# Kernel optimization log

Hardware: AMD Instinct MI355X
Metric: run time of the kernel (lower is better)

## Reference

```python
import jax, jax.numpy as jnp
import numpy as np

NUM_PER_SCALE = (64, 64, 64)   # static num_intervals_per_scale
DIST_BINS = 21
NUM_CLASSES = 5
D = 128   # node_embedding_dim
N = 512   # number of nodes (time frames)
KSIZE = 5


def _gru_last(x_seq, lens, Wih, Whh, bih, bhh):
    """Masked GRU over padded seqs; final hidden at each sequence's true length.
    x_seq: [I, T, F], lens: [I]. PyTorch GRU cell math."""
    I, T, _ = x_seq.shape
    H = Whh.shape[1]
    mask_t = (jnp.arange(T)[None, :] < lens[:, None]).T  # [T, I]

    def step(h, inp):
        x_t, m = inp
        gi = x_t @ Wih.T + bih            # [I, 3H]
        gh = h @ Whh.T + bhh
        ir, iz, in_ = jnp.split(gi, 3, axis=-1)
        hr, hz, hn = jnp.split(gh, 3, axis=-1)
        r = jax.nn.sigmoid(ir + hr)
        z = jax.nn.sigmoid(iz + hz)
        n = jnp.tanh(in_ + r * hn)
        h_new = (1.0 - z) * n + z * h
        return jnp.where(m[:, None], h_new, h), None

    h0 = jnp.zeros((I, H), x_seq.dtype)
    h_fin, _ = jax.lax.scan(step, h0, (jnp.swapaxes(x_seq, 0, 1), mask_t))
    return h_fin


def _bigru_last(x_pad, lens, Wih, Whh, bih, bhh):
    """Bidirectional GRU final hiddens, matching packed-sequence semantics."""
    hf = _gru_last(x_pad, lens, Wih[0], Whh[0], bih[0], bhh[0])
    T = x_pad.shape[1]
    t = jnp.arange(T)[None, :]
    rev = jnp.where(t < lens[:, None], lens[:, None] - 1 - t, t)  # reverse within valid length
    x_rev = jnp.take_along_axis(x_pad, rev[:, :, None], axis=1)
    hb = _gru_last(x_rev, lens, Wih[1], Whh[1], bih[1], bhh[1])
    return hf, hb


def reference(node_embeddings, time_positions, node_pred, audio_len,
              cur_anchor_intervals, smooth_kernel,
              feat_Wih, feat_Whh, feat_bih, feat_bhh,
              abn_Wih, abn_Whh, abn_bih, abn_bhh,
              start_w, end_w,
              uni_W1, uni_b1, uni_W2, uni_b2, uni_W3, uni_b3):
    n, d = node_embeddings.shape
    al = audio_len
    # temporal encoding
    freqs = jnp.linspace(0.0, 10.0, d)
    x = node_embeddings + 0.05 * jnp.sin(time_positions * freqs)  # [N, D]
    # grouped gaussian smoothing over time per class channel (symmetric kernel)
    pad = KSIZE // 2
    xp = jnp.pad(node_pred, ((pad, pad), (0, 0)))
    win = jnp.stack([xp[k:k + n] for k in range(KSIZE)])          # [K, N, C]
    smoothed = jax.nn.softmax(jnp.einsum('k,knc->nc', smooth_kernel, win), axis=-1)
    abnormal = smoothed[:, 0]                                     # normal_class_idx = 0
    tpos = time_positions[:, 0] * al                              # [N]

    bounds_list, conf_list, cls_list = [], [], []
    off = 0
    for s in range(3):
        ni = NUM_PER_SCALE[s]
        anc = cur_anchor_intervals[off:off + ni]
        off += ni
        starts, ends = anc[:, 0], anc[:, 1]
        mask = (tpos[None, :] >= starts[:, None]) & (tpos[None, :] <= ends[:, None])  # [ni, N]
        lens = mask.sum(axis=1)
        # stable gather: in-interval nodes first, original node order preserved
        key = jnp.where(mask, 0, n) + jnp.arange(n)[None, :]
        order = jnp.argsort(key, axis=1)
        x_pad = x[order]                       # [ni, N, D]
        abn_pad = abnormal[order][:, :, None]  # [ni, N, 1]
        hf, hb = _bigru_last(x_pad, lens, feat_Wih[s], feat_Whh[s], feat_bih[s], feat_bhh[s])
        af, ab = _bigru_last(abn_pad, lens, abn_Wih[s], abn_Whh[s], abn_bih[s], abn_bhh[s])
        local_feat = jnp.concatenate([hf, hb], axis=1)             # [ni, 2D]
        local_abn = (af[:, 0] + ab[:, 0]) * 0.5
        centers = (starts + ends) * 0.5
        widths = ends - starts
        sf = jnp.concatenate([local_feat, local_abn[:, None],
                              (centers / al)[:, None], (widths / al)[:, None]], axis=1)
        h = jax.nn.relu(sf @ uni_W1[s] + uni_b1[s])
        h = jax.nn.relu(h @ uni_W2[s] + uni_b2[s])   # dropout inactive (eval)
        out = h @ uni_W3[s] + uni_b3[s]
        sl = out[:, :DIST_BINS]
        el = out[:, DIST_BINS:2 * DIST_BINS]
        conf = out[:, 2 * DIST_BINS]
        cls = out[:, 2 * DIST_BINS + 1:]
        so = jax.nn.softmax(sl, axis=1) @ start_w[s]
        eo = jax.nn.softmax(el, axis=1) @ end_w[s]
        st = jnp.clip(starts + so, 0.0, al)
        en = jnp.clip(ends + eo, 0.0, al)
        bounds_list.append(jnp.stack([st, en], axis=1))
        conf_list.append(conf)
        cls_list.append(cls)
    return (jnp.concatenate(bounds_list, 0),
            jnp.concatenate(conf_list, 0),
            jnp.concatenate(cls_list, 0))


def setup_inputs():
    key = jax.random.key(0)
    ks = jax.random.split(key, 16)
    node_embeddings = jax.random.normal(ks[0], (N, D), dtype=jnp.float32)
    time_positions = jax.random.uniform(ks[1], (N, 1), dtype=jnp.float32)
    node_pred = jax.random.normal(ks[2], (N, NUM_CLASSES), dtype=jnp.float32)
    audio_len = jnp.ones((), jnp.float32)
    total = sum(NUM_PER_SCALE)
    st = jax.random.uniform(ks[3], (total,), minval=0.0, maxval=0.75)
    wd = jax.random.uniform(ks[4], (total,), minval=0.05, maxval=0.2)
    cur_anchor_intervals = jnp.stack([st, jnp.minimum(st + wd, 1.0)], axis=1)
    smooth_kernel = jnp.array([0.06136, 0.24477, 0.38774, 0.24477, 0.06136], jnp.float32)
    feat_Wih = 0.05 * jax.random.normal(ks[5], (3, 2, 3 * D, D))
    feat_Whh = 0.05 * jax.random.normal(ks[6], (3, 2, 3 * D, D))
    feat_bih = 0.05 * jax.random.normal(ks[7], (3, 2, 3 * D))
    feat_bhh = 0.05 * jax.random.normal(ks[8], (3, 2, 3 * D))
    abn_Wih = 0.5 * jax.random.normal(ks[9], (3, 2, 3, 1))
    abn_Whh = 0.5 * jax.random.normal(ks[10], (3, 2, 3, 1))
    abn_bih = 0.5 * jax.random.normal(ks[11], (3, 2, 3))
    abn_bhh = 0.5 * jax.random.normal(ks[12], (3, 2, 3))
    lin = jnp.linspace(-20.0, 20.0, DIST_BINS)
    start_w = jnp.tile(lin[None, :], (3, 1))
    end_w = jnp.tile(lin[None, :], (3, 1))
    fin = 2 * D + 3
    fout = 2 * DIST_BINS + 1 + (NUM_CLASSES - 1)
    uni_W1 = jax.random.normal(ks[13], (3, fin, 256)) / float(np.sqrt(fin))
    uni_b1 = jnp.zeros((3, 256), jnp.float32)
    uni_W2 = jax.random.normal(ks[14], (3, 256, 256)) / 16.0
    uni_b2 = jnp.zeros((3, 256), jnp.float32)
    uni_W3 = jax.random.normal(ks[15], (3, 256, fout)) / 16.0
    uni_b3 = jnp.zeros((3, fout), jnp.float32)
    return dict(node_embeddings=node_embeddings, time_positions=time_positions,
                node_pred=node_pred, audio_len=audio_len,
                cur_anchor_intervals=cur_anchor_intervals, smooth_kernel=smooth_kernel,
                feat_Wih=feat_Wih, feat_Whh=feat_Whh, feat_bih=feat_bih, feat_bhh=feat_bhh,
                abn_Wih=abn_Wih, abn_Whh=abn_Whh, abn_bih=abn_bih, abn_bhh=abn_bhh,
                start_w=start_w, end_w=end_w,
                uni_W1=uni_W1, uni_b1=uni_b1, uni_W2=uni_W2, uni_b2=uni_b2,
                uni_W3=uni_W3, uni_b3=uni_b3)
```

## Files before the change

kernel.cpp:

```cpp
#include <hip/hip_runtime.h>
#include <math.h>

#define N_NODES 512
#define DIM 128
#define NANCH 192
#define G3 384
#define FOUT 47
#define DBINS 21

__device__ __forceinline__ float fast_sigmoid(float x) {
    return __builtin_amdgcn_rcpf(1.f + __expf(-x));
}
__device__ __forceinline__ float fast_tanh(float x) {
    return 1.f - 2.f * __builtin_amdgcn_rcpf(1.f + __expf(2.f * x));
}

__global__ __launch_bounds__(384) void prep_kernel(
    const float* __restrict__ emb, const float* __restrict__ tpin,
    const float* __restrict__ Wih, const float* __restrict__ bih,
    const float* __restrict__ alp, const float* __restrict__ anchors,
    const float* __restrict__ npred, const float* __restrict__ skern,
    const float* __restrict__ aWih, const float* __restrict__ aWhh,
    const float* __restrict__ abih, const float* __restrict__ abhh,
    float* __restrict__ xW, int* __restrict__ members,
    int* __restrict__ lens, float* __restrict__ abn_res)
{
    int blk = blockIdx.x;
    int tid = threadIdx.x;
    if (blk < 192) {
        int sd = blk >> 5;
        int ng = blk & 31;
        __shared__ __align__(16) float xs[16][DIM];
        for (int idx = tid; idx < 16 * DIM; idx += 384) {
            int m = idx >> 7, k = idx & 127;
            int node = ng * 16 + m;
            float tv = tpin[node];
            float freq = 10.f * (float)k / 127.f;
            xs[m][k] = emb[node * DIM + k] + 0.05f * __sinf(tv * freq);
        }
        __syncthreads();
        float acc[16];
        float b = bih[sd * G3 + tid];
        #pragma unroll
        for (int m = 0; m < 16; ++m) acc[m] = b;
        const float* wrow = Wih + ((size_t)sd * G3 + tid) * DIM;
        for (int k = 0; k < DIM; k += 4) {
            float4 w4 = *(const float4*)(wrow + k);
            #pragma unroll
            for (int m = 0; m < 16; ++m) {
                float4 xv = *(const float4*)&xs[m][k];
                acc[m] = fmaf(w4.x, xv.x, acc[m]);
                acc[m] = fmaf(w4.y, xv.y, acc[m]);
                acc[m] = fmaf(w4.z, xv.z, acc[m]);
                acc[m] = fmaf(w4.w, xv.w, acc[m]);
            }
        }
        #pragma unroll
        for (int m = 0; m < 16; ++m)
            xW[((size_t)sd * N_NODES + ng * 16 + m) * G3 + tid] = acc[m];
    } else {
        int a = blk - 192;
        float al = alp[0];
        float s0 = anchors[a * 2 + 0];
        float e0 = anchors[a * 2 + 1];
        __shared__ int memloc[N_NODES];
        __shared__ float abn_lds[N_NODES];
        for (int node = tid; node < N_NODES; node += 384) {
            float sc[5];
            #pragma unroll
            for (int ch = 0; ch < 5; ++ch) {
                float acc = 0.f;
                #pragma unroll
                for (int k = 0; k < 5; ++k) {
                    int r = node + k - 2;
                    if (r >= 0 && r < N_NODES) acc += skern[k] * npred[r * 5 + ch];
                }
                sc[ch] = acc;
            }
            float m = sc[0];
            #pragma unroll
            for (int ch = 1; ch < 5; ++ch) m = fmaxf(m, sc[ch]);
            float sum = 0.f;
            #pragma unroll
            for (int ch = 0; ch < 5; ++ch) sum += __expf(sc[ch] - m);
            abn_lds[node] = __expf(sc[0] - m) / sum;
        }
        __syncthreads();
        if (tid < 64) {
            int lane = tid;
            int count = 0;
            for (int c = 0; c < N_NODES / 64; ++c) {
                int node = c * 64 + lane;
                float tp = tpin[node] * al;
                bool in = (tp >= s0) && (tp <= e0);
                unsigned long long m = __ballot(in);
                if (in) {
                    int pos = count + __popcll(m & ((1ull << lane) - 1ull));
                    members[a * N_NODES + pos] = node;
                    memloc[pos] = node;
                }
                count += __popcll(m);
            }
            if (lane == 0) lens[a] = count;
            int sc3 = a >> 6;
            float h = 0.f;
            if (lane < 2) {
                int sd = sc3 * 2 + lane;
                float wi0 = aWih[sd*3+0], wi1 = aWih[sd*3+1], wi2 = aWih[sd*3+2];
                float wh0 = aWhh[sd*3+0], wh1 = aWhh[sd*3+1], wh2 = aWhh[sd*3+2];
                float bi0 = abih[sd*3+0], bi1 = abih[sd*3+1], bi2 = abih[sd*3+2];
                float bh0 = abhh[sd*3+0], bh1 = abhh[sd*3+1], bh2 = abhh[sd*3+2];
                for (int t = 0; t < count; ++t) {
                    int idx = lane ? (count - 1 - t) : t;
                    float xv = abn_lds[memloc[idx]];
                    float r = fast_sigmoid(fmaf(wi0, xv, bi0) + fmaf(wh0, h, bh0));
                    float z = fast_sigmoid(fmaf(wi1, xv, bi1) + fmaf(wh1, h, bh1));
                    float nv = fast_tanh(fmaf(wi2, xv, bi2) + r * fmaf(wh2, h, bh2));
                    h = (1.f - z) * nv + z * h;
                }
            }
            float hb = __shfl(h, 1);
            if (lane == 0) abn_res[a] = 0.5f * (h + hb);
        }
    }
}

__global__ __launch_bounds__(512, 2) void gru_feat_kernel(
    const float* __restrict__ xW, const float* __restrict__ Whh,
    const float* __restrict__ bhh, const int* __restrict__ members,
    const int* __restrict__ lens, float* __restrict__ feat_out)
{
    int b = blockIdx.x;
    int a = b >> 1;
    int dir = b & 1;
    int s3 = a >> 6;
    int sd = s3 * 2 + dir;
    int t0 = threadIdx.x;
    int j  = t0 >> 2;
    int s  = t0 & 3;

    float wr[32], wz[32], wn[32];
    {
        const float* base = Whh + ((size_t)sd * G3) * DIM;
        const float* pr = base + (size_t)(j        ) * DIM + s * 32;
        const float* pz = base + (size_t)(j + DIM  ) * DIM + s * 32;
        const float* pn = base + (size_t)(j + 2*DIM) * DIM + s * 32;
        #pragma unroll
        for (int q = 0; q < 8; ++q) {
            float4 v = *(const float4*)(pr + 4 * q);
            wr[4*q+0]=v.x; wr[4*q+1]=v.y; wr[4*q+2]=v.z; wr[4*q+3]=v.w;
        }
        #pragma unroll
        for (int q = 0; q < 8; ++q) {
            float4 v = *(const float4*)(pz + 4 * q);
            wz[4*q+0]=v.x; wz[4*q+1]=v.y; wz[4*q+2]=v.z; wz[4*q+3]=v.w;
        }
        #pragma unroll
        for (int q = 0; q < 8; ++q) {
            float4 v = *(const float4*)(pn + 4 * q);
            wn[4*q+0]=v.x; wn[4*q+1]=v.y; wn[4*q+2]=v.z; wn[4*q+3]=v.w;
        }
    }
    float bhr = bhh[sd * G3 + j];
    float bhz = bhh[sd * G3 + DIM + j];
    float bhn = bhh[sd * G3 + 2 * DIM + j];

    const float* xWp = xW + (size_t)sd * N_NODES * G3;
    const int* mem = members + a * N_NODES;
    int len = lens[a];

    __shared__ __align__(16) float hbuf[2][4][36];
    for (int i = t0; i < 2 * 4 * 36; i += 512) ((float*)hbuf)[i] = 0.f;
    __syncthreads();

    int node0 = (len > 0) ? mem[dir ? (len - 1) : 0] : 0;
    float gr = xWp[(size_t)node0 * G3 + j];
    float gz = xWp[(size_t)node0 * G3 + DIM + j];
    float gn = xWp[(size_t)node0 * G3 + 2 * DIM + j];

    int cur = 0;
    for (int t = 0; t < len; ++t) {
        float gr_n = 0.f, gz_n = 0.f, gn_n = 0.f;
        if (t + 1 < len) {
            int nn = mem[dir ? (len - 2 - t) : (t + 1)];
            gr_n = xWp[(size_t)nn * G3 + j];
            gz_n = xWp[(size_t)nn * G3 + DIM + j];
            gn_n = xWp[(size_t)nn * G3 + 2 * DIM + j];
        }
        float ar = 0.f, az = 0.f, an_ = 0.f;
        const float4* hp = (const float4*)(&hbuf[cur][s][0]);
        #pragma unroll
        for (int q = 0; q < 8; ++q) {
            float4 hv = hp[q];
            ar = fmaf(wr[4*q+0], hv.x, ar); ar = fmaf(wr[4*q+1], hv.y, ar);
            ar = fmaf(wr[4*q+2], hv.z, ar); ar = fmaf(wr[4*q+3], hv.w, ar);
            az = fmaf(wz[4*q+0], hv.x, az); az = fmaf(wz[4*q+1], hv.y, az);
            az = fmaf(wz[4*q+2], hv.z, az); az = fmaf(wz[4*q+3], hv.w, az);
            an_ = fmaf(wn[4*q+0], hv.x, an_); an_ = fmaf(wn[4*q+1], hv.y, an_);
            an_ = fmaf(wn[4*q+2], hv.z, an_); an_ = fmaf(wn[4*q+3], hv.w, an_);
        }
        ar  += __shfl_xor(ar, 1);  ar  += __shfl_xor(ar, 2);
        az  += __shfl_xor(az, 1);  az  += __shfl_xor(az, 2);
        an_ += __shfl_xor(an_, 1); an_ += __shfl_xor(an_, 2);

        float r  = fast_sigmoid(gr + ar + bhr);
        float z  = fast_sigmoid(gz + az + bhz);
        float nv = fast_tanh(gn + r * (an_ + bhn));
        float hj = hbuf[cur][j >> 5][j & 31];
        float hnew = (1.f - z) * nv + z * hj;
        if (s == 0) hbuf[cur ^ 1][j >> 5][j & 31] = hnew;
        __syncthreads();
        cur ^= 1;
        gr = gr_n; gz = gz_n; gn = gn_n;
    }
    if (s == 0) feat_out[a * 256 + dir * DIM + j] = hbuf[cur][j >> 5][j & 31];
}

__global__ __launch_bounds__(256) void head_kernel(
    const float* __restrict__ feat, const float* __restrict__ abn_res,
    const float* __restrict__ anchors, const float* __restrict__ alp,
    const float* __restrict__ W1, const float* __restrict__ b1,
    const float* __restrict__ W2, const float* __restrict__ b2,
    const float* __restrict__ W3, const float* __restrict__ b3,
    const float* __restrict__ sw, const float* __restrict__ ew,
    float* __restrict__ out)
{
    int a = blockIdx.x;
    int tid = threadIdx.x;
    int s = a >> 6;
    __shared__ float sf[260];
    __shared__ float h1[256];
    __shared__ float h2[256];
    __shared__ float o[FOUT];
    float al = alp[0];
    float st = anchors[a * 2 + 0];
    float en = anchors[a * 2 + 1];
    sf[tid] = feat[a * 256 + tid];
    if (tid == 0) {
        sf[256] = abn_res[a];
        sf[257] = (st + en) * 0.5f / al;
        sf[258] = (en - st) / al;
    }
    __syncthreads();

    const float* w1 = W1 + (size_t)s * 259 * 256;
    float acc = b1[s * 256 + tid];
    for (int jj = 0; jj < 259; ++jj) acc = fmaf(sf[jj], w1[jj * 256 + tid], acc);
    h1[tid] = fmaxf(acc, 0.f);
    __syncthreads();

    const float* w2 = W2 + (size_t)s * 256 * 256;
    acc = b2[s * 256 + tid];
    for (int jj = 0; jj < 256; ++jj) acc = fmaf(h1[jj], w2[jj * 256 + tid], acc);
    h2[tid] = fmaxf(acc, 0.f);
    __syncthreads();

    if (tid < FOUT) {
        const float* w3 = W3 + (size_t)s * 256 * FOUT;
        acc = b3[s * FOUT + tid];
        for (int jj = 0; jj < 256; ++jj) acc = fmaf(h2[jj], w3[jj * FOUT + tid], acc);
        o[tid] = acc;
    }
    __syncthreads();

    if (tid < 2) {
        const float* lw = (tid == 0) ? (sw + s * DBINS) : (ew + s * DBINS);
        const float* sl = o + tid * DBINS;
        float m = sl[0];
        for (int jj = 1; jj < DBINS; ++jj) m = fmaxf(m, sl[jj]);
        float sum = 0.f, dot = 0.f;
        for (int jj = 0; jj < DBINS; ++jj) {
            float e = __expf(sl[jj] - m);
            sum += e;
            dot = fmaf(e, lw[jj], dot);
        }
        float off = dot / sum;
        float base = (tid == 0) ? st : en;
        out[a * 2 + tid] = fminf(fmaxf(base + off, 0.f), al);
    }
    if (tid == 42) out[2 * NANCH + a] = o[42];
    if (tid >= 43 && tid < FOUT) out[3 * NANCH + a * 4 + (tid - 43)] = o[tid];
}

extern "C" void kernel_launch(void* const* d_in, const int* in_sizes, int n_in,
                              void* d_out, int out_size, void* d_ws, size_t ws_size,
                              hipStream_t stream) {
    const float* emb   = (const float*)d_in[0];
    const float* tpin  = (const float*)d_in[1];
    const float* npred = (const float*)d_in[2];
    const float* alp   = (const float*)d_in[3];
    const float* anch  = (const float*)d_in[4];
    const float* skern = (const float*)d_in[5];
    const float* fWih  = (const float*)d_in[6];
    const float* fWhh  = (const float*)d_in[7];
    const float* fbih  = (const float*)d_in[8];
    const float* fbhh  = (const float*)d_in[9];
    const float* aWih  = (const float*)d_in[10];
    const float* aWhh  = (const float*)d_in[11];
    const float* abih  = (const float*)d_in[12];
    const float* abhh  = (const float*)d_in[13];
    const float* sw    = (const float*)d_in[14];
    const float* ew    = (const float*)d_in[15];
    const float* W1    = (const float*)d_in[16];
    const float* b1    = (const float*)d_in[17];
    const float* W2    = (const float*)d_in[18];
    const float* b2    = (const float*)d_in[19];
    const float* W3    = (const float*)d_in[20];
    const float* b3    = (const float*)d_in[21];

    float* ws = (float*)d_ws;
    float* xW       = ws;
    float* abn_res  = ws + 1179648;
    float* feat     = ws + 1179904;
    int*   members  = (int*)(ws + 1229056);
    int*   lens     = (int*)(ws + 1327360);
    float* outp     = (float*)d_out;

    prep_kernel<<<384, 384, 0, stream>>>(emb, tpin, fWih, fbih, alp, anch, npred, skern,
                                         aWih, aWhh, abih, abhh,
                                         xW, members, lens, abn_res);
    gru_feat_kernel<<<2 * NANCH, 512, 0, stream>>>(xW, fWhh, fbhh, members, lens, feat);
    head_kernel<<<NANCH, 256, 0, stream>>>(feat, abn_res, anch, alp,
                                           W1, b1, W2, b2, W3, b3, sw, ew, outp);
}
```

Measured before the change: 252.4 us.

## Process two anchors per GRU block to reuse recurrent weights in registers

Each GRU block now runs two anchor sequences (same scale and direction) together, reusing the register-resident Whh weights for both hidden-state matvecs. This halves the grid to 192 blocks and gives each thread more independent FMA chains, while member index lists are staged into shared memory. The loop runs to the longer of the two lengths and masks updates for the shorter one, so the two lengths going unequal wastes work. The halved block count may also leave many compute units idle.

```diff
diff --git a/kernel.cpp b/kernel.cpp
--- a/kernel.cpp
+++ b/kernel.cpp
@@ -131,89 +131,131 @@
     const int* __restrict__ lens, float* __restrict__ feat_out)
 {
     int b = blockIdx.x;
-    int a = b >> 1;
+    int pr = b >> 1;
     int dir = b & 1;
-    int s3 = a >> 6;
+    int aA = pr * 2, aB = aA + 1;
+    int s3 = aA >> 6;
     int sd = s3 * 2 + dir;
     int t0 = threadIdx.x;
     int j  = t0 >> 2;
     int s  = t0 & 3;
 
+    __shared__ __align__(16) float hbuf[2][2][4][36];
+    __shared__ int memA[N_NODES], memB[N_NODES];
+
+    int lenA = lens[aA], lenB = lens[aB];
+    int len = max(lenA, lenB);
+    for (int i = t0; i < 2 * 2 * 4 * 36; i += 512) ((float*)hbuf)[i] = 0.f;
+    for (int i = t0; i < lenA; i += 512) memA[i] = members[aA * N_NODES + i];
+    for (int i = t0; i < lenB; i += 512) memB[i] = members[aB * N_NODES + i];
+
     float wr[32], wz[32], wn[32];
     {
         const float* base = Whh + ((size_t)sd * G3) * DIM;
-        const float* pr = base + (size_t)(j        ) * DIM + s * 32;
-        const float* pz = base + (size_t)(j + DIM  ) * DIM + s * 32;
-        const float* pn = base + (size_t)(j + 2*DIM) * DIM + s * 32;
+        const float* pr_ = base + (size_t)(j        ) * DIM + s * 32;
+        const float* pz_ = base + (size_t)(j + DIM  ) * DIM + s * 32;
+        const float* pn_ = base + (size_t)(j + 2*DIM) * DIM + s * 32;
         #pragma unroll
         for (int q = 0; q < 8; ++q) {
-            float4 v = *(const float4*)(pr + 4 * q);
+            float4 v = *(const float4*)(pr_ + 4 * q);
             wr[4*q+0]=v.x; wr[4*q+1]=v.y; wr[4*q+2]=v.z; wr[4*q+3]=v.w;
         }
         #pragma unroll
         for (int q = 0; q < 8; ++q) {
-            float4 v = *(const float4*)(pz + 4 * q);
+            float4 v = *(const float4*)(pz_ + 4 * q);
             wz[4*q+0]=v.x; wz[4*q+1]=v.y; wz[4*q+2]=v.z; wz[4*q+3]=v.w;
         }
         #pragma unroll
         for (int q = 0; q < 8; ++q) {
-            float4 v = *(const float4*)(pn + 4 * q);
+            float4 v = *(const float4*)(pn_ + 4 * q);
             wn[4*q+0]=v.x; wn[4*q+1]=v.y; wn[4*q+2]=v.z; wn[4*q+3]=v.w;
         }
     }
     float bhr = bhh[sd * G3 + j];
     float bhz = bhh[sd * G3 + DIM + j];
     float bhn = bhh[sd * G3 + 2 * DIM + j];
-
     const float* xWp = xW + (size_t)sd * N_NODES * G3;
-    const int* mem = members + a * N_NODES;
-    int len = lens[a];
-
-    __shared__ __align__(16) float hbuf[2][4][36];
-    for (int i = t0; i < 2 * 4 * 36; i += 512) ((float*)hbuf)[i] = 0.f;
-    __syncthreads();
-
-    int node0 = (len > 0) ? mem[dir ? (len - 1) : 0] : 0;
-    float gr = xWp[(size_t)node0 * G3 + j];
-    float gz = xWp[(size_t)node0 * G3 + DIM + j];
-    float gn = xWp[(size_t)node0 * G3 + 2 * DIM + j];
+    __syncthreads();
+
+    int nA = (lenA > 0) ? memA[dir ? (lenA - 1) : 0] : 0;
+    int nB = (lenB > 0) ? memB[dir ? (lenB - 1) : 0] : 0;
+    float grA = xWp[(size_t)nA * G3 + j];
+    float gzA = xWp[(size_t)nA * G3 + DIM + j];
+    float gnA = xWp[(size_t)nA * G3 + 2 * DIM + j];
+    float grB = xWp[(size_t)nB * G3 + j];
+    float gzB = xWp[(size_t)nB * G3 + DIM + j];
+    float gnB = xWp[(size_t)nB * G3 + 2 * DIM + j];
 
     int cur = 0;
-    for (int t = 0; t < len; ++t) {
-        float gr_n = 0.f, gz_n = 0.f, gn_n = 0.f;
-        if (t + 1 < len) {
-            int nn = mem[dir ? (len - 2 - t) : (t + 1)];
-            gr_n = xWp[(size_t)nn * G3 + j];
-            gz_n = xWp[(size_t)nn * G3 + DIM + j];
-            gn_n = xWp[(size_t)nn * G3 + 2 * DIM + j];
-        }
-        float ar = 0.f, az = 0.f, an_ = 0.f;
-        const float4* hp = (const float4*)(&hbuf[cur][s][0]);
+    for (int tt = 0; tt < len; ++tt) {
+        float grA_n = 0.f, gzA_n = 0.f, gnA_n = 0.f;
+        float grB_n = 0.f, gzB_n = 0.f, gnB_n = 0.f;
+        int t1 = tt + 1;
+        if (t1 < lenA) {
+            int nn = memA[dir ? (lenA - 1 - t1) : t1];
+            grA_n = xWp[(size_t)nn * G3 + j];
+            gzA_n = xWp[(size_t)nn * G3 + DIM + j];
+            gnA_n = xWp[(size_t)nn * G3 + 2 * DIM + j];
+        }
+        if (t1 < lenB) {
+            int nn = memB[dir ? (lenB - 1 - t1) : t1];
+            grB_n = xWp[(size_t)nn * G3 + j];
+            gzB_n = xWp[(size_t)nn * G3 + DIM + j];
+            gnB_n = xWp[(size_t)nn * G3 + 2 * DIM + j];
+        }
+        float arA = 0.f, azA = 0.f, anA = 0.f;
+        float arB = 0.f, azB = 0.f, anB = 0.f;
+        const float4* hpA = (const float4*)(&hbuf[cur][0][s][0]);
+        const float4* hpB = (const float4*)(&hbuf[cur][1][s][0]);
         #pragma unroll
         for (int q = 0; q < 8; ++q) {
-            float4 hv = hp[q];
-            ar = fmaf(wr[4*q+0], hv.x, ar); ar = fmaf(wr[4*q+1], hv.y, ar);
-            ar = fmaf(wr[4*q+2], hv.z, ar); ar = fmaf(wr[4*q+3], hv.w, ar);
-            az = fmaf(wz[4*q+0], hv.x, az); az = fmaf(wz[4*q+1], hv.y, az);
-            az = fmaf(wz[4*q+2], hv.z, az); az = fmaf(wz[4*q+3], hv.w, az);
-            an_ = fmaf(wn[4*q+0], hv.x, an_); an_ = fmaf(wn[4*q+1], hv.y, an_);
-            an_ = fmaf(wn[4*q+2], hv.z, an_); an_ = fmaf(wn[4*q+3], hv.w, an_);
-        }
-        ar  += __shfl_xor(ar, 1);  ar  += __shfl_xor(ar, 2);
-        az  += __shfl_xor(az, 1);  az  += __shfl_xor(az, 2);
-        an_ += __shfl_xor(an_, 1); an_ += __shfl_xor(an_, 2);
-
-        float r  = fast_sigmoid(gr + ar + bhr);
-        float z  = fast_sigmoid(gz + az + bhz);
-        float nv = fast_tanh(gn + r * (an_ + bhn));
-        float hj = hbuf[cur][j >> 5][j & 31];
-        float hnew = (1.f - z) * nv + z * hj;
-        if (s == 0) hbuf[cur ^ 1][j >> 5][j & 31] = hnew;
+            float4 hA = hpA[q];
+            float4 hB = hpB[q];
+            arA = fmaf(wr[4*q+0], hA.x, arA); arB = fmaf(wr[4*q+0], hB.x, arB);
+            arA = fmaf(wr[4*q+1], hA.y, arA); arB = fmaf(wr[4*q+1], hB.y, arB);
+            arA = fmaf(wr[4*q+2], hA.z, arA); arB = fmaf(wr[4*q+2], hB.z, arB);
+            arA = fmaf(wr[4*q+3], hA.w, arA); arB = fmaf(wr[4*q+3], hB.w, arB);
+            azA = fmaf(wz[4*q+0], hA.x, azA); azB = fmaf(wz[4*q+0], hB.x, azB);
+            azA = fmaf(wz[4*q+1], hA.y, azA); azB = fmaf(wz[4*q+1], hB.y, azB);
+            azA = fmaf(wz[4*q+2], hA.z, azA); azB = fmaf(wz[4*q+2], hB.z, azB);
+            azA = fmaf(wz[4*q+3], hA.w, azA); azB = fmaf(wz[4*q+3], hB.w, azB);
+            anA = fmaf(wn[4*q+0], hA.x, anA); anB = fmaf(wn[4*q+0], hB.x, anB);
+            anA = fmaf(wn[4*q+1], hA.y, anA); anB = fmaf(wn[4*q+1], hB.y, anB);
+            anA = fmaf(wn[4*q+2], hA.z, anA); anB = fmaf(wn[4*q+2], hB.z, anB);
+            anA = fmaf(wn[4*q+3], hA.w, anA); anB = fmaf(wn[4*q+3], hB.w, anB);
+        }
+        arA += __shfl_xor(arA, 1); arA += __shfl_xor(arA, 2);
+        azA += __shfl_xor(azA, 1); azA += __shfl_xor(azA, 2);
+        anA += __shfl_xor(anA, 1); anA += __shfl_xor(anA, 2);
+        arB += __shfl_xor(arB, 1); arB += __shfl_xor(arB, 2);
+        azB += __shfl_xor(azB, 1); azB += __shfl_xor(azB, 2);
+        anB += __shfl_xor(anB, 1); anB += __shfl_xor(anB, 2);
+
+        float rA  = fast_sigmoid(grA + arA + bhr);
+        float zA  = fast_sigmoid(gzA + azA + bhz);
+        float nvA = fast_tanh(gnA + rA * (anA + bhn));
+        float hjA = hbuf[cur][0][j >> 5][j & 31];
+        float hA2 = (tt < lenA) ? ((1.f - zA) * nvA + zA * hjA) : hjA;
+
+        float rB  = fast_sigmoid(grB + arB + bhr);
+        float zB  = fast_sigmoid(gzB + azB + bhz);
+        float nvB = fast_tanh(gnB + rB * (anB + bhn));
+        float hjB = hbuf[cur][1][j >> 5][j & 31];
+        float hB2 = (tt < lenB) ? ((1.f - zB) * nvB + zB * hjB) : hjB;
+
+        if (s == 0) {
+            hbuf[cur ^ 1][0][j >> 5][j & 31] = hA2;
+            hbuf[cur ^ 1][1][j >> 5][j & 31] = hB2;
+        }
         __syncthreads();
         cur ^= 1;
-        gr = gr_n; gz = gz_n; gn = gn_n;
-    }
-    if (s == 0) feat_out[a * 256 + dir * DIM + j] = hbuf[cur][j >> 5][j & 31];
+        grA = grA_n; gzA = gzA_n; gnA = gnA_n;
+        grB = grB_n; gzB = gzB_n; gnB = gnB_n;
+    }
+    if (s == 0) {
+        feat_out[aA * 256 + dir * DIM + j] = hbuf[cur][0][j >> 5][j & 31];
+        feat_out[aB * 256 + dir * DIM + j] = hbuf[cur][1][j >> 5][j & 31];
+    }
 }
 
 __global__ __launch_bounds__(256) void head_kernel(
@@ -319,7 +361,7 @@
     prep_kernel<<<384, 384, 0, stream>>>(emb, tpin, fWih, fbih, alp, anch, npred, skern,
                                          aWih, aWhh, abih, abhh,
                                          xW, members, lens, abn_res);
-    gru_feat_kernel<<<2 * NANCH, 512, 0, stream>>>(xW, fWhh, fbhh, members, lens, feat);
+    gru_feat_kernel<<<NANCH, 512, 0, stream>>>(xW, fWhh, fbhh, members, lens, feat);
     head_kernel<<<NANCH, 256, 0, stream>>>(feat, abn_res, anch, alp,
                                            W1, b1, W2, b2, W3, b3, sw, ew, outp);
 }
```

New measurement: 283.7 us. 12.4% more time.

## Fuse MLP head into GRU kernel via last-block-done atomic flag

Applied to the files above, without the earlier changes.

Removes the separate head kernel launch: each GRU block increments a per-anchor counter after writing its direction's hidden state, and the second block to finish for an anchor runs the three-layer MLP head and output writes. Flags are reset in the prep kernel. This saves a kernel launch and the gap between launches. In exchange it adds threadfences and an atomic, and makes the last-finishing block do serial head work while other blocks may already be done.

```diff
diff --git a/kernel.cpp b/kernel.cpp
--- a/kernel.cpp
+++ b/kernel.cpp
@@ -23,7 +23,8 @@
     const float* __restrict__ aWih, const float* __restrict__ aWhh,
     const float* __restrict__ abih, const float* __restrict__ abhh,
     float* __restrict__ xW, int* __restrict__ members,
-    int* __restrict__ lens, float* __restrict__ abn_res)
+    int* __restrict__ lens, float* __restrict__ abn_res,
+    int* __restrict__ flags)
 {
     int blk = blockIdx.x;
     int tid = threadIdx.x;
@@ -60,6 +61,7 @@
             xW[((size_t)sd * N_NODES + ng * 16 + m) * G3 + tid] = acc[m];
     } else {
         int a = blk - 192;
+        if (tid == 0) flags[a] = 0;
         float al = alp[0];
         float s0 = anchors[a * 2 + 0];
         float e0 = anchors[a * 2 + 1];
@@ -128,7 +130,14 @@
 __global__ __launch_bounds__(512, 2) void gru_feat_kernel(
     const float* __restrict__ xW, const float* __restrict__ Whh,
     const float* __restrict__ bhh, const int* __restrict__ members,
-    const int* __restrict__ lens, float* __restrict__ feat_out)
+    const int* __restrict__ lens, float* __restrict__ feat_out,
+    int* __restrict__ flags, const float* __restrict__ abn_res,
+    const float* __restrict__ anchors, const float* __restrict__ alp,
+    const float* __restrict__ W1, const float* __restrict__ b1,
+    const float* __restrict__ W2, const float* __restrict__ b2,
+    const float* __restrict__ W3, const float* __restrict__ b3,
+    const float* __restrict__ sw, const float* __restrict__ ew,
+    float* __restrict__ out)
 {
     int b = blockIdx.x;
     int a = b >> 1;
@@ -214,20 +223,17 @@
         gr = gr_n; gz = gz_n; gn = gn_n;
     }
     if (s == 0) feat_out[a * 256 + dir * DIM + j] = hbuf[cur][j >> 5][j & 31];
-}
-
-__global__ __launch_bounds__(256) void head_kernel(
-    const float* __restrict__ feat, const float* __restrict__ abn_res,
-    const float* __restrict__ anchors, const float* __restrict__ alp,
-    const float* __restrict__ W1, const float* __restrict__ b1,
-    const float* __restrict__ W2, const float* __restrict__ b2,
-    const float* __restrict__ W3, const float* __restrict__ b3,
-    const float* __restrict__ sw, const float* __restrict__ ew,
-    float* __restrict__ out)
-{
-    int a = blockIdx.x;
-    int tid = threadIdx.x;
-    int s = a >> 6;
+
+    __syncthreads();
+    __shared__ int winner;
+    if (t0 == 0) {
+        __threadfence();
+        winner = atomicAdd(&flags[a], 1);
+    }
+    __syncthreads();
+    if (winner != 1) return;
+    __threadfence();
+
     __shared__ float sf[260];
     __shared__ float h1[256];
     __shared__ float h2[256];
@@ -235,37 +241,38 @@
     float al = alp[0];
     float st = anchors[a * 2 + 0];
     float en = anchors[a * 2 + 1];
-    sf[tid] = feat[a * 256 + tid];
-    if (tid == 0) {
+    if (t0 < 256) sf[t0] = feat_out[a * 256 + t0];
+    if (t0 == 0) {
         sf[256] = abn_res[a];
         sf[257] = (st + en) * 0.5f / al;
         sf[258] = (en - st) / al;
     }
     __syncthreads();
 
-    const float* w1 = W1 + (size_t)s * 259 * 256;
-    float acc = b1[s * 256 + tid];
-    for (int jj = 0; jj < 259; ++jj) acc = fmaf(sf[jj], w1[jj * 256 + tid], acc);
-    h1[tid] = fmaxf(acc, 0.f);
-    __syncthreads();
-
-    const float* w2 = W2 + (size_t)s * 256 * 256;
-    acc = b2[s * 256 + tid];
-    for (int jj = 0; jj < 256; ++jj) acc = fmaf(h1[jj], w2[jj * 256 + tid], acc);
-    h2[tid] = fmaxf(acc, 0.f);
-    __syncthreads();
-
-    if (tid < FOUT) {
-        const float* w3 = W3 + (size_t)s * 256 * FOUT;
-        acc = b3[s * FOUT + tid];
-        for (int jj = 0; jj < 256; ++jj) acc = fmaf(h2[jj], w3[jj * FOUT + tid], acc);
-        o[tid] = acc;
-    }
-    __syncthreads();
-
-    if (tid < 2) {
-        const float* lw = (tid == 0) ? (sw + s * DBINS) : (ew + s * DBINS);
-        const float* sl = o + tid * DBINS;
+    if (t0 < 256) {
+        const float* w1 = W1 + (size_t)s3 * 259 * 256;
+        float acc = b1[s3 * 256 + t0];
+        for (int jj = 0; jj < 259; ++jj) acc = fmaf(sf[jj], w1[jj * 256 + t0], acc);
+        h1[t0] = fmaxf(acc, 0.f);
+    }
+    __syncthreads();
+    if (t0 < 256) {
+        const float* w2 = W2 + (size_t)s3 * 256 * 256;
+        float acc = b2[s3 * 256 + t0];
+        for (int jj = 0; jj < 256; ++jj) acc = fmaf(h1[jj], w2[jj * 256 + t0], acc);
+        h2[t0] = fmaxf(acc, 0.f);
+    }
+    __syncthreads();
+    if (t0 < FOUT) {
+        const float* w3 = W3 + (size_t)s3 * 256 * FOUT;
+        float acc = b3[s3 * FOUT + t0];
+        for (int jj = 0; jj < 256; ++jj) acc = fmaf(h2[jj], w3[jj * FOUT + t0], acc);
+        o[t0] = acc;
+    }
+    __syncthreads();
+    if (t0 < 2) {
+        const float* lw = (t0 == 0) ? (sw + s3 * DBINS) : (ew + s3 * DBINS);
+        const float* sl = o + t0 * DBINS;
         float m = sl[0];
         for (int jj = 1; jj < DBINS; ++jj) m = fmaxf(m, sl[jj]);
         float sum = 0.f, dot = 0.f;
@@ -275,11 +282,11 @@
             dot = fmaf(e, lw[jj], dot);
         }
         float off = dot / sum;
-        float base = (tid == 0) ? st : en;
-        out[a * 2 + tid] = fminf(fmaxf(base + off, 0.f), al);
-    }
-    if (tid == 42) out[2 * NANCH + a] = o[42];
-    if (tid >= 43 && tid < FOUT) out[3 * NANCH + a * 4 + (tid - 43)] = o[tid];
+        float base = (t0 == 0) ? st : en;
+        out[a * 2 + t0] = fminf(fmaxf(base + off, 0.f), al);
+    }
+    if (t0 == 42) out[2 * NANCH + a] = o[42];
+    if (t0 >= 43 && t0 < FOUT) out[3 * NANCH + a * 4 + (t0 - 43)] = o[t0];
 }
 
 extern "C" void kernel_launch(void* const* d_in, const int* in_sizes, int n_in,
@@ -314,12 +321,13 @@
     float* feat     = ws + 1179904;
     int*   members  = (int*)(ws + 1229056);
     int*   lens     = (int*)(ws + 1327360);
+    int*   flags    = (int*)(ws + 1327616);
     float* outp     = (float*)d_out;
 
     prep_kernel<<<384, 384, 0, stream>>>(emb, tpin, fWih, fbih, alp, anch, npred, skern,
                                          aWih, aWhh, abih, abhh,
-                                         xW, members, lens, abn_res);
-    gru_feat_kernel<<<2 * NANCH, 512, 0, stream>>>(xW, fWhh, fbhh, members, lens, feat);
-    head_kernel<<<NANCH, 256, 0, stream>>>(feat, abn_res, anch, alp,
-                                           W1, b1, W2, b2, W3, b3, sw, ew, outp);
-}
+                                         xW, members, lens, abn_res, flags);
+    gru_feat_kernel<<<2 * NANCH, 512, 0, stream>>>(xW, fWhh, fbhh, members, lens, feat,
+                                                   flags, abn_res, anch, alp,
+                                                   W1, b1, W2, b2, W3, b3, sw, ew, outp);
+}
```

Result: slower. 266.9 us (+5.8%).
